# Optimization experiments

Measured on AMD Instinct MI355X. Metric: run time of the kernel, lower is better.

## Reference

```python
import jax, jax.numpy as jnp
import numpy as np

EPS = 1e-5

def _ln(x, g, b):
    mu = jnp.mean(x, axis=-1, keepdims=True)
    var = jnp.mean((x - mu) ** 2, axis=-1, keepdims=True)
    return (x - mu) * jax.lax.rsqrt(var + EPS) * g + b

def _lin(x, W, b):
    return x @ W + b

def setup_inputs() -> dict:
    B, D_IN, H = 32768, 512, 512
    key = jax.random.key(0)
    ks = jax.random.split(key, 20)
    def W(k, din, dout):
        return jax.random.normal(k, (din, dout), jnp.float32) / np.sqrt(din)
    inp = {
        'x': jax.random.normal(ks[0], (B, D_IN), jnp.float32),
        'h_prev': jax.random.normal(ks[1], (B, H), jnp.float32),
        's_prev': jax.random.normal(ks[2], (B, H), jnp.float32),
        'W_in': W(ks[3], D_IN, H), 'b_in': jnp.zeros((H,), jnp.float32),
        'g_ln_in': jnp.ones((H,), jnp.float32), 'b_ln_in': jnp.zeros((H,), jnp.float32),
        'g_ln_r': jnp.ones((H,), jnp.float32), 'b_ln_r': jnp.zeros((H,), jnp.float32),
        'g_ln_z': jnp.ones((H,), jnp.float32), 'b_ln_z': jnp.zeros((H,), jnp.float32),
        'g_ln_h': jnp.ones((H,), jnp.float32), 'b_ln_h': jnp.zeros((H,), jnp.float32),
        'W_r': W(ks[4], H, H), 'b_r': jnp.zeros((H,), jnp.float32),
        'W_z': W(ks[5], H, H), 'b_z': jnp.zeros((H,), jnp.float32),
        'W_k': W(ks[6], H, H), 'b_k': jnp.zeros((H,), jnp.float32),
        'W_v': W(ks[7], H, H), 'b_v': jnp.zeros((H,), jnp.float32),
        'W_h': W(ks[8], H, H), 'b_h': jnp.zeros((H,), jnp.float32),
        'W_d': W(ks[9], H, H), 'b_d': jnp.zeros((H,), jnp.float32),
    }
    return inp

def reference(x, h_prev, s_prev, W_in, b_in, g_ln_in, b_ln_in,
              g_ln_r, b_ln_r, g_ln_z, b_ln_z, g_ln_h, b_ln_h,
              W_r, b_r, W_z, b_z, W_k, b_k, W_v, b_v, W_h, b_h, W_d, b_d):
    # u = LN(input_proj(x))
    u = _ln(_lin(x, W_in, b_in), g_ln_in, b_ln_in)
    r = jax.nn.sigmoid(_ln(_lin(u, W_r, b_r), g_ln_r, b_ln_r))  # computed as in original (unused downstream)
    z = jax.nn.sigmoid(_ln(_lin(u, W_z, b_z), g_ln_z, b_ln_z))
    k = _lin(u, W_k, b_k)
    v = _lin(u, W_v, b_v)
    decay = jax.nn.sigmoid(_lin(u, W_d, b_d))
    s = decay * s_prev + k * v
    c = jnp.tanh(_ln(_lin(u + s, W_h, b_h), g_ln_h, b_ln_h))
    h = (1.0 - z) * c + z * h_prev
    return (h, s)
```

## Files before the change

kernel.cpp:

```cpp
#include <hip/hip_runtime.h>

typedef __attribute__((ext_vector_type(8))) short bf16x8;
typedef __attribute__((ext_vector_type(4))) float f32x4;

#define LN_EPS 1e-5f
#define MSZ ((size_t)32768 * 512)
#define WSZ ((size_t)512 * 512)

typedef const __attribute__((address_space(1))) void* gptr_t;
typedef __attribute__((address_space(3))) void* lptr_t;

__device__ __forceinline__ float b2f(unsigned short h) {
    unsigned int u = ((unsigned int)h) << 16;
    return __uint_as_float(u);
}
__device__ __forceinline__ short f2b(float f) {
    unsigned int u = __float_as_uint(f);
    unsigned int r = (u + 0x7FFFu + ((u >> 16) & 1u)) >> 16;
    return (short)(unsigned short)r;
}
__device__ __forceinline__ float sigmoid_f(float x) {
    return 1.0f / (1.0f + __expf(-x));
}
__device__ __forceinline__ float ldS(const void* p, size_t i, int isbf) {
    return isbf ? b2f(((const unsigned short*)p)[i]) : ((const float*)p)[i];
}
__device__ __forceinline__ void ld8(const void* p, size_t i, int isbf, float* o) {
    if (isbf) {
        bf16x8 v = *(const bf16x8*)((const unsigned short*)p + i);
        #pragma unroll
        for (int j = 0; j < 8; ++j) o[j] = b2f((unsigned short)v[j]);
    } else {
        f32x4 a = *(const f32x4*)((const float*)p + i);
        f32x4 b = *(const f32x4*)((const float*)p + i + 4);
        #pragma unroll
        for (int j = 0; j < 4; ++j) { o[j] = a[j]; o[4 + j] = b[j]; }
    }
}

__global__ void detect_dtype(const unsigned int* __restrict__ ones, int* __restrict__ flag) {
    if (threadIdx.x == 0 && blockIdx.x == 0)
        *flag = (ones[0] == 0x3F803F80u) ? 1 : 0;
}

__global__ __launch_bounds__(256) void transpose6(
    const void* __restrict__ s0, const void* __restrict__ s1,
    const void* __restrict__ s2, const void* __restrict__ s3,
    const void* __restrict__ s4, const void* __restrict__ s5,
    unsigned short* __restrict__ d0, unsigned short* __restrict__ d1,
    unsigned short* __restrict__ d2, unsigned short* __restrict__ d3,
    unsigned short* __restrict__ d4, unsigned short* __restrict__ d5,
    const int* __restrict__ flagp)
{
    const int isbf = *flagp;
    const void* srcs[6] = {s0, s1, s2, s3, s4, s5};
    unsigned short* dsts[6] = {d0, d1, d2, d3, d4, d5};
    const void* src = srcs[blockIdx.z];
    unsigned short* dst = dsts[blockIdx.z];

    __shared__ unsigned short tile[32][33];
    int tx = threadIdx.x, ty = threadIdx.y;
    int colbase = blockIdx.x * 32;
    int rowbase = blockIdx.y * 32;
    #pragma unroll
    for (int i = 0; i < 32; i += 8)
        tile[ty + i][tx] = (unsigned short)f2b(
            ldS(src, (size_t)(rowbase + ty + i) * 512 + colbase + tx, isbf));
    __syncthreads();
    #pragma unroll
    for (int i = 0; i < 32; i += 8)
        dst[(size_t)(colbase + ty + i) * 512 + rowbase + tx] = tile[tx][ty + i];
}

__global__ __launch_bounds__(256) void gemm_bt(
    const void* __restrict__ A,
    const unsigned short* __restrict__ BT,
    const void* __restrict__ bias0, const void* __restrict__ bias1,
    unsigned short* __restrict__ C0, unsigned short* __restrict__ C1,
    int nbshift, const int* __restrict__ flagp, int op, int araw,
    const void* __restrict__ s_prev,
    const unsigned short* __restrict__ kvb,
    const unsigned short* __restrict__ ubuf,
    void* __restrict__ dout)
{
    const int isbf = *flagp;
    const int K = 512;
    __shared__ unsigned short smem[128 * 136];
    unsigned short* As = smem;
    unsigned short* Bs = smem + 128 * 64;

    int t = threadIdx.x;
    int lane = t & 63;
    int wave = t >> 6;
    int wm = (wave >> 1) * 64;
    int wn = (wave & 1) * 64;

    int bflat = blockIdx.x;
    int xcd = bflat & 7;
    int bi = bflat >> 3;
    int n0 = (bi & ((1 << nbshift) - 1)) << 7;
    int mi = bi >> nbshift;
    int m0 = ((xcd << 5) + mi) << 7;

    int lr = lane >> 3;
    int lg = lane & 7;
    int gsrc = lg ^ lr;
    const unsigned short* Ab = (const unsigned short*)A;

    size_t a_off[4], b_off[4];
    #pragma unroll
    for (int i = 0; i < 4; ++i) {
        int c = wave * 4 + i;
        a_off[i] = (size_t)(m0 + 8 * c + lr) * K + gsrc * 8;
        b_off[i] = (size_t)(n0 + 8 * c + lr) * K + gsrc * 8;
    }

    int ml = lane & 15;
    int kg = lane >> 4;
    int sw = ml & 7;

    f32x4 acc[4][4] = {};

    const int doConv = (araw && !isbf);

    for (int k0 = 0; k0 < K; k0 += 64) {
        if (doConv) {
            const float* Af = (const float*)A;
            int r = t >> 1;
            #pragma unroll
            for (int j = 0; j < 4; ++j) {
                int G = (t & 1) * 4 + j;
                size_t gi = (size_t)(m0 + r) * K + k0 + G * 8;
                f32x4 lo = *(const f32x4*)&Af[gi];
                f32x4 hi = *(const f32x4*)&Af[gi + 4];
                bf16x8 p;
                #pragma unroll
                for (int z = 0; z < 4; ++z) { p[z] = f2b(lo[z]); p[4 + z] = f2b(hi[z]); }
                *(bf16x8*)&As[r * 64 + ((G ^ (r & 7)) * 8)] = p;
            }
        } else {
            #pragma unroll
            for (int i = 0; i < 4; ++i) {
                int c = wave * 4 + i;
                __builtin_amdgcn_global_load_lds(
                    (gptr_t)(const void*)(Ab + a_off[i] + k0),
                    (lptr_t)(void*)(As + c * 512), 16, 0, 0);
            }
        }
        #pragma unroll
        for (int i = 0; i < 4; ++i) {
            int c = wave * 4 + i;
            __builtin_amdgcn_global_load_lds(
                (gptr_t)(const void*)(BT + b_off[i] + k0),
                (lptr_t)(void*)(Bs + c * 512), 16, 0, 0);
        }
        __syncthreads();

        #pragma unroll
        for (int ks = 0; ks < 2; ++ks) {
            bf16x8 af[4], bfr[4];
            #pragma unroll
            for (int i = 0; i < 4; ++i) {
                int ga = ((ks << 2) + kg) ^ sw;
                af[i]  = *(const bf16x8*)&As[(wm + i * 16 + ml) * 64 + ga * 8];
                bfr[i] = *(const bf16x8*)&Bs[(wn + i * 16 + ml) * 64 + ga * 8];
            }
            #pragma unroll
            for (int i = 0; i < 4; ++i)
                #pragma unroll
                for (int j = 0; j < 4; ++j)
                    acc[i][j] = __builtin_amdgcn_mfma_f32_16x16x32_bf16(
                        af[i], bfr[j], acc[i][j], 0, 0, 0);
        }
        __syncthreads();
    }

    int seg = n0 >> 9;
    const void* bias = seg ? bias1 : bias0;
    unsigned short* Cs = seg ? C1 : C0;
    int ncol0 = n0 & 511;
    int cq = lane >> 4;
    int cl = lane & 15;
    #pragma unroll
    for (int j = 0; j < 4; ++j) {
        float bv = ldS(bias, ncol0 + wn + j * 16 + cl, isbf);
        #pragma unroll
        for (int i = 0; i < 4; ++i) {
            #pragma unroll
            for (int r = 0; r < 4; ++r) {
                float v = acc[i][j][r] + bv;
                if (op == 2) v = sigmoid_f(v);
                smem[(wm + i * 16 + cq * 4 + r) * 136 + wn + j * 16 + cl] =
                    (unsigned short)f2b(v);
            }
        }
    }
    __syncthreads();

    int tr = t >> 4;
    int tc = (t & 15) * 8;
    #pragma unroll
    for (int it = 0; it < 8; ++it) {
        int rl = it * 16 + tr;
        size_t idx = (size_t)(m0 + rl) * 512 + ncol0 + tc;
        bf16x8 v8 = *(bf16x8*)&smem[rl * 136 + tc];
        if (op == 0) {
            *(bf16x8*)&Cs[idx] = v8;
        } else if (op == 1) {
            bf16x8 k8 = *(const bf16x8*)&Cs[idx];
            bf16x8 o;
            #pragma unroll
            for (int z = 0; z < 8; ++z)
                o[z] = f2b(b2f((unsigned short)v8[z]) * b2f((unsigned short)k8[z]));
            *(bf16x8*)&Cs[idx] = o;
        } else {
            float sp[8];
            ld8(s_prev, idx, isbf, sp);
            bf16x8 kv8 = *(const bf16x8*)&kvb[idx];
            bf16x8 u8  = *(const bf16x8*)&ubuf[idx];
            float sv[8];
            bf16x8 a8;
            #pragma unroll
            for (int z = 0; z < 8; ++z) {
                sv[z] = b2f((unsigned short)v8[z]) * sp[z] + b2f((unsigned short)kv8[z]);
                a8[z] = f2b(b2f((unsigned short)u8[z]) + sv[z]);
            }
            if (isbf) {
                bf16x8 s8;
                #pragma unroll
                for (int z = 0; z < 8; ++z) s8[z] = f2b(sv[z]);
                *(bf16x8*)&((unsigned short*)dout)[MSZ + idx] = s8;
            } else {
                f32x4 lo, hi;
                #pragma unroll
                for (int z = 0; z < 4; ++z) { lo[z] = sv[z]; hi[z] = sv[4 + z]; }
                *(f32x4*)&((float*)dout)[MSZ + idx] = lo;
                *(f32x4*)&((float*)dout)[MSZ + idx + 4] = hi;
            }
            *(bf16x8*)&((unsigned short*)dout)[idx] = a8;
        }
    }
}

__global__ __launch_bounds__(256) void ln_rows(
    const unsigned short* __restrict__ X,
    const void* __restrict__ g,
    const void* __restrict__ b,
    unsigned short* __restrict__ Y,
    const int* __restrict__ flagp)
{
    const int isbf = *flagp;
    int wave = threadIdx.x >> 6, lane = threadIdx.x & 63;
    size_t row = (size_t)blockIdx.x * 4 + wave;
    size_t base = row * 512 + (size_t)lane * 8;

    bf16x8 xv = *(const bf16x8*)&X[base];
    float x[8];
    float s = 0.f, s2 = 0.f;
    #pragma unroll
    for (int i = 0; i < 8; ++i) {
        x[i] = b2f((unsigned short)xv[i]);
        s += x[i]; s2 += x[i] * x[i];
    }
    #pragma unroll
    for (int off = 32; off > 0; off >>= 1) {
        s  += __shfl_xor(s, off);
        s2 += __shfl_xor(s2, off);
    }
    float mu = s * (1.f / 512.f);
    float var = s2 * (1.f / 512.f) - mu * mu;
    float rs = rsqrtf(var + LN_EPS);

    float gv[8], bv[8];
    ld8(g, (size_t)lane * 8, isbf, gv);
    ld8(b, (size_t)lane * 8, isbf, bv);
    bf16x8 o;
    #pragma unroll
    for (int i = 0; i < 8; ++i)
        o[i] = f2b((x[i] - mu) * rs * gv[i] + bv[i]);
    *(bf16x8*)&Y[base] = o;
}

__global__ __launch_bounds__(256) void fused_out(
    const unsigned short* __restrict__ hlin,
    const unsigned short* __restrict__ zlin,
    const void* __restrict__ h_prev,
    const void* __restrict__ g_z, const void* __restrict__ b_z,
    const void* __restrict__ g_h, const void* __restrict__ b_h,
    void* __restrict__ dout,
    const int* __restrict__ flagp)
{
    const int isbf = *flagp;
    int wave = threadIdx.x >> 6, lane = threadIdx.x & 63;
    size_t row = (size_t)blockIdx.x * 4 + wave;
    size_t base = row * 512 + (size_t)lane * 8;

    bf16x8 zv8 = *(const bf16x8*)&zlin[base];
    bf16x8 hv8 = *(const bf16x8*)&hlin[base];
    float zf[8], hf[8];
    float sz = 0.f, sz2 = 0.f, sh = 0.f, sh2 = 0.f;
    #pragma unroll
    for (int i = 0; i < 8; ++i) {
        zf[i] = b2f((unsigned short)zv8[i]);
        hf[i] = b2f((unsigned short)hv8[i]);
        sz += zf[i]; sz2 += zf[i] * zf[i];
        sh += hf[i]; sh2 += hf[i] * hf[i];
    }
    #pragma unroll
    for (int off = 32; off > 0; off >>= 1) {
        sz  += __shfl_xor(sz, off);  sz2 += __shfl_xor(sz2, off);
        sh  += __shfl_xor(sh, off);  sh2 += __shfl_xor(sh2, off);
    }
    float muz = sz * (1.f / 512.f);
    float rsz = rsqrtf(sz2 * (1.f / 512.f) - muz * muz + LN_EPS);
    float muh = sh * (1.f / 512.f);
    float rsh = rsqrtf(sh2 * (1.f / 512.f) - muh * muh + LN_EPS);

    float gz[8], bz[8], gh[8], bh[8], hp[8];
    ld8(g_z, (size_t)lane * 8, isbf, gz);
    ld8(b_z, (size_t)lane * 8, isbf, bz);
    ld8(g_h, (size_t)lane * 8, isbf, gh);
    ld8(b_h, (size_t)lane * 8, isbf, bh);
    ld8(h_prev, base, isbf, hp);

    float hout[8];
    #pragma unroll
    for (int i = 0; i < 8; ++i) {
        float z = sigmoid_f((zf[i] - muz) * rsz * gz[i] + bz[i]);
        float c = tanhf((hf[i] - muh) * rsh * gh[i] + bh[i]);
        hout[i] = (1.f - z) * c + z * hp[i];
    }
    if (isbf) {
        bf16x8 o;
        #pragma unroll
        for (int i = 0; i < 8; ++i) o[i] = f2b(hout[i]);
        *(bf16x8*)&((unsigned short*)dout)[base] = o;
    } else {
        f32x4 a, b;
        #pragma unroll
        for (int i = 0; i < 4; ++i) { a[i] = hout[i]; b[i] = hout[4 + i]; }
        *(f32x4*)&((float*)dout)[base] = a;
        *(f32x4*)&((float*)dout)[base + 4] = b;
    }
}

extern "C" void kernel_launch(void* const* d_in, const int* in_sizes, int n_in,
                              void* d_out, int out_size, void* d_ws, size_t ws_size,
                              hipStream_t stream)
{
    (void)in_sizes; (void)n_in; (void)out_size; (void)ws_size;

    const void* x       = d_in[0];
    const void* h_prev  = d_in[1];
    const void* s_prev  = d_in[2];
    const void* W_in    = d_in[3];
    const void* b_in    = d_in[4];
    const void* g_ln_in = d_in[5];
    const void* b_ln_in = d_in[6];
    const void* g_ln_z  = d_in[9];
    const void* b_ln_z  = d_in[10];
    const void* g_ln_h  = d_in[11];
    const void* b_ln_h  = d_in[12];
    const void* W_z     = d_in[15];
    const void* b_z     = d_in[16];
    const void* W_k     = d_in[17];
    const void* b_k     = d_in[18];
    const void* W_v     = d_in[19];
    const void* b_v     = d_in[20];
    const void* W_h     = d_in[21];
    const void* b_h     = d_in[22];
    const void* W_d     = d_in[23];
    const void* b_d     = d_in[24];

    unsigned short* ws = (unsigned short*)d_ws;
    unsigned short* U  = ws;
    unsigned short* L  = ws + MSZ;
    unsigned short* Kb = ws + 2 * MSZ;
    unsigned short* WT = ws + 3 * MSZ;
    unsigned short* WT_in = WT;
    unsigned short* WT_z  = WT + 1 * WSZ;
    unsigned short* WT_k  = WT + 2 * WSZ;
    unsigned short* WT_v  = WT + 3 * WSZ;
    unsigned short* WT_d  = WT + 4 * WSZ;
    unsigned short* WT_h  = WT + 5 * WSZ;
    int* flag = (int*)(WT + 6 * WSZ);

    detect_dtype<<<1, 64, 0, stream>>>((const unsigned int*)g_ln_in, flag);
    transpose6<<<dim3(16, 16, 6), dim3(32, 8), 0, stream>>>(
        W_in, W_z, W_k, W_v, W_d, W_h,
        WT_in, WT_z, WT_k, WT_v, WT_d, WT_h, flag);

    gemm_bt<<<1024, 256, 0, stream>>>(x, WT_in, b_in, nullptr, L, nullptr,
                                      2, flag, 0, 1,
                                      nullptr, nullptr, nullptr, nullptr);
    ln_rows<<<8192, 256, 0, stream>>>(L, g_ln_in, b_ln_in, U, flag);
    gemm_bt<<<2048, 256, 0, stream>>>(U, WT_z, b_z, b_k, L, Kb,
                                      3, flag, 0, 0,
                                      nullptr, nullptr, nullptr, nullptr);
    gemm_bt<<<1024, 256, 0, stream>>>(U, WT_v, b_v, nullptr, Kb, nullptr,
                                      2, flag, 1, 0,
                                      nullptr, nullptr, nullptr, nullptr);
    gemm_bt<<<1024, 256, 0, stream>>>(U, WT_d, b_d, nullptr, nullptr, nullptr,
                                      2, flag, 2, 0,
                                      s_prev, Kb, U, d_out);
    gemm_bt<<<1024, 256, 0, stream>>>(d_out, WT_h, b_h, nullptr, Kb, nullptr,
                                      2, flag, 0, 0,
                                      nullptr, nullptr, nullptr, nullptr);
    fused_out<<<8192, 256, 0, stream>>>(Kb, L, h_prev,
                                        g_ln_z, b_ln_z, g_ln_h, b_ln_h,
                                        d_out, flag);
}
```

Measured before the change: 539.9 us.

## Merge z/k/v/d GEMMs into one launch and split elementwise state update

Moves the fp32-to-bf16 conversion of x into a separate pre-pass kernel, so the GEMM always uses the direct global-to-LDS load path. The four projections z, k, v and d are computed in a single wide GEMM launch (N=2048) writing to four buffers, replacing three launches that had fused epilogues. The decay sigmoid, the state update s and the u+s computation move into a standalone elementwise kernel. This cuts launches and reuses the A tiles, at the cost of extra bf16 intermediate traffic (V and D buffers written and read back, plus the converted x).

```diff
diff --git a/kernel.cpp b/kernel.cpp
--- a/kernel.cpp
+++ b/kernel.cpp
@@ -72,22 +72,36 @@
         dst[(size_t)(colbase + ty + i) * 512 + rowbase + tx] = tile[tx][ty + i];
 }
 
+__global__ __launch_bounds__(256) void cvt_x(
+    const float* __restrict__ x, unsigned short* __restrict__ Xb,
+    const int* __restrict__ flagp)
+{
+    if (*flagp) return;
+    size_t i = ((size_t)blockIdx.x * 256 + threadIdx.x) * 8;
+    f32x4 a = *(const f32x4*)&x[i];
+    f32x4 b = *(const f32x4*)&x[i + 4];
+    bf16x8 o;
+    #pragma unroll
+    for (int j = 0; j < 4; ++j) { o[j] = f2b(a[j]); o[4 + j] = f2b(b[j]); }
+    *(bf16x8*)&Xb[i] = o;
+}
+
 __global__ __launch_bounds__(256) void gemm_bt(
-    const void* __restrict__ A,
+    const void* __restrict__ Araw, const unsigned short* __restrict__ Aconv,
     const unsigned short* __restrict__ BT,
-    const void* __restrict__ bias0, const void* __restrict__ bias1,
+    const void* __restrict__ b0, const void* __restrict__ b1,
+    const void* __restrict__ b2, const void* __restrict__ b3,
     unsigned short* __restrict__ C0, unsigned short* __restrict__ C1,
-    int nbshift, const int* __restrict__ flagp, int op, int araw,
-    const void* __restrict__ s_prev,
-    const unsigned short* __restrict__ kvb,
-    const unsigned short* __restrict__ ubuf,
-    void* __restrict__ dout)
+    unsigned short* __restrict__ C2, unsigned short* __restrict__ C3,
+    int nbshift, const int* __restrict__ flagp)
 {
     const int isbf = *flagp;
     const int K = 512;
     __shared__ unsigned short smem[128 * 136];
     unsigned short* As = smem;
     unsigned short* Bs = smem + 128 * 64;
+
+    const unsigned short* Ab = isbf ? (const unsigned short*)Araw : Aconv;
 
     int t = threadIdx.x;
     int lane = t & 63;
@@ -105,7 +119,6 @@
     int lr = lane >> 3;
     int lg = lane & 7;
     int gsrc = lg ^ lr;
-    const unsigned short* Ab = (const unsigned short*)A;
 
     size_t a_off[4], b_off[4];
     #pragma unroll
@@ -121,31 +134,13 @@
 
     f32x4 acc[4][4] = {};
 
-    const int doConv = (araw && !isbf);
-
     for (int k0 = 0; k0 < K; k0 += 64) {
-        if (doConv) {
-            const float* Af = (const float*)A;
-            int r = t >> 1;
-            #pragma unroll
-            for (int j = 0; j < 4; ++j) {
-                int G = (t & 1) * 4 + j;
-                size_t gi = (size_t)(m0 + r) * K + k0 + G * 8;
-                f32x4 lo = *(const f32x4*)&Af[gi];
-                f32x4 hi = *(const f32x4*)&Af[gi + 4];
-                bf16x8 p;
-                #pragma unroll
-                for (int z = 0; z < 4; ++z) { p[z] = f2b(lo[z]); p[4 + z] = f2b(hi[z]); }
-                *(bf16x8*)&As[r * 64 + ((G ^ (r & 7)) * 8)] = p;
-            }
-        } else {
-            #pragma unroll
-            for (int i = 0; i < 4; ++i) {
-                int c = wave * 4 + i;
-                __builtin_amdgcn_global_load_lds(
-                    (gptr_t)(const void*)(Ab + a_off[i] + k0),
-                    (lptr_t)(void*)(As + c * 512), 16, 0, 0);
-            }
+        #pragma unroll
+        for (int i = 0; i < 4; ++i) {
+            int c = wave * 4 + i;
+            __builtin_amdgcn_global_load_lds(
+                (gptr_t)(const void*)(Ab + a_off[i] + k0),
+                (lptr_t)(void*)(As + c * 512), 16, 0, 0);
         }
         #pragma unroll
         for (int i = 0; i < 4; ++i) {
@@ -176,8 +171,8 @@
     }
 
     int seg = n0 >> 9;
-    const void* bias = seg ? bias1 : bias0;
-    unsigned short* Cs = seg ? C1 : C0;
+    const void* bias = (seg == 0) ? b0 : (seg == 1) ? b1 : (seg == 2) ? b2 : b3;
+    unsigned short* Cs = (seg == 0) ? C0 : (seg == 1) ? C1 : (seg == 2) ? C2 : C3;
     int ncol0 = n0 & 511;
     int cq = lane >> 4;
     int cl = lane & 15;
@@ -188,10 +183,8 @@
         for (int i = 0; i < 4; ++i) {
             #pragma unroll
             for (int r = 0; r < 4; ++r) {
-                float v = acc[i][j][r] + bv;
-                if (op == 2) v = sigmoid_f(v);
                 smem[(wm + i * 16 + cq * 4 + r) * 136 + wn + j * 16 + cl] =
-                    (unsigned short)f2b(v);
+                    (unsigned short)f2b(acc[i][j][r] + bv);
             }
         }
     }
@@ -203,43 +196,49 @@
     for (int it = 0; it < 8; ++it) {
         int rl = it * 16 + tr;
         size_t idx = (size_t)(m0 + rl) * 512 + ncol0 + tc;
-        bf16x8 v8 = *(bf16x8*)&smem[rl * 136 + tc];
-        if (op == 0) {
-            *(bf16x8*)&Cs[idx] = v8;
-        } else if (op == 1) {
-            bf16x8 k8 = *(const bf16x8*)&Cs[idx];
-            bf16x8 o;
-            #pragma unroll
-            for (int z = 0; z < 8; ++z)
-                o[z] = f2b(b2f((unsigned short)v8[z]) * b2f((unsigned short)k8[z]));
-            *(bf16x8*)&Cs[idx] = o;
-        } else {
-            float sp[8];
-            ld8(s_prev, idx, isbf, sp);
-            bf16x8 kv8 = *(const bf16x8*)&kvb[idx];
-            bf16x8 u8  = *(const bf16x8*)&ubuf[idx];
-            float sv[8];
-            bf16x8 a8;
-            #pragma unroll
-            for (int z = 0; z < 8; ++z) {
-                sv[z] = b2f((unsigned short)v8[z]) * sp[z] + b2f((unsigned short)kv8[z]);
-                a8[z] = f2b(b2f((unsigned short)u8[z]) + sv[z]);
-            }
-            if (isbf) {
-                bf16x8 s8;
-                #pragma unroll
-                for (int z = 0; z < 8; ++z) s8[z] = f2b(sv[z]);
-                *(bf16x8*)&((unsigned short*)dout)[MSZ + idx] = s8;
-            } else {
-                f32x4 lo, hi;
-                #pragma unroll
-                for (int z = 0; z < 4; ++z) { lo[z] = sv[z]; hi[z] = sv[4 + z]; }
-                *(f32x4*)&((float*)dout)[MSZ + idx] = lo;
-                *(f32x4*)&((float*)dout)[MSZ + idx + 4] = hi;
-            }
-            *(bf16x8*)&((unsigned short*)dout)[idx] = a8;
-        }
-    }
+        *(bf16x8*)&Cs[idx] = *(bf16x8*)&smem[rl * 136 + tc];
+    }
+}
+
+__global__ __launch_bounds__(256) void fused_sa(
+    const unsigned short* __restrict__ klin,
+    const unsigned short* __restrict__ vlin,
+    const unsigned short* __restrict__ dlin,
+    const unsigned short* __restrict__ u,
+    const void* __restrict__ s_prev,
+    void* __restrict__ dout,
+    const int* __restrict__ flagp)
+{
+    const int isbf = *flagp;
+    size_t i = ((size_t)blockIdx.x * 256 + threadIdx.x) * 8;
+    bf16x8 k8 = *(const bf16x8*)&klin[i];
+    bf16x8 v8 = *(const bf16x8*)&vlin[i];
+    bf16x8 d8 = *(const bf16x8*)&dlin[i];
+    bf16x8 u8 = *(const bf16x8*)&u[i];
+    float sp[8];
+    ld8(s_prev, i, isbf, sp);
+
+    float sv[8];
+    bf16x8 a8;
+    #pragma unroll
+    for (int z = 0; z < 8; ++z) {
+        float dv = sigmoid_f(b2f((unsigned short)d8[z]));
+        sv[z] = dv * sp[z] + b2f((unsigned short)k8[z]) * b2f((unsigned short)v8[z]);
+        a8[z] = f2b(b2f((unsigned short)u8[z]) + sv[z]);
+    }
+    if (isbf) {
+        bf16x8 s8;
+        #pragma unroll
+        for (int z = 0; z < 8; ++z) s8[z] = f2b(sv[z]);
+        *(bf16x8*)&((unsigned short*)dout)[MSZ + i] = s8;
+    } else {
+        f32x4 lo, hi;
+        #pragma unroll
+        for (int z = 0; z < 4; ++z) { lo[z] = sv[z]; hi[z] = sv[4 + z]; }
+        *(f32x4*)&((float*)dout)[MSZ + i] = lo;
+        *(f32x4*)&((float*)dout)[MSZ + i + 4] = hi;
+    }
+    *(bf16x8*)&((unsigned short*)dout)[i] = a8;
 }
 
 __global__ __launch_bounds__(256) void ln_rows(
@@ -376,7 +375,9 @@
     unsigned short* U  = ws;
     unsigned short* L  = ws + MSZ;
     unsigned short* Kb = ws + 2 * MSZ;
-    unsigned short* WT = ws + 3 * MSZ;
+    unsigned short* Vb = ws + 3 * MSZ;
+    unsigned short* Db = ws + 4 * MSZ;
+    unsigned short* WT = ws + 5 * MSZ;
     unsigned short* WT_in = WT;
     unsigned short* WT_z  = WT + 1 * WSZ;
     unsigned short* WT_k  = WT + 2 * WSZ;
@@ -390,22 +391,23 @@
         W_in, W_z, W_k, W_v, W_d, W_h,
         WT_in, WT_z, WT_k, WT_v, WT_d, WT_h, flag);
 
-    gemm_bt<<<1024, 256, 0, stream>>>(x, WT_in, b_in, nullptr, L, nullptr,
-                                      2, flag, 0, 1,
-                                      nullptr, nullptr, nullptr, nullptr);
+    cvt_x<<<8192, 256, 0, stream>>>((const float*)x, Vb, flag);
+
+    gemm_bt<<<1024, 256, 0, stream>>>(x, Vb, WT_in,
+                                      b_in, b_in, b_in, b_in,
+                                      L, L, L, L, 2, flag);
     ln_rows<<<8192, 256, 0, stream>>>(L, g_ln_in, b_ln_in, U, flag);
-    gemm_bt<<<2048, 256, 0, stream>>>(U, WT_z, b_z, b_k, L, Kb,
-                                      3, flag, 0, 0,
-                                      nullptr, nullptr, nullptr, nullptr);
-    gemm_bt<<<1024, 256, 0, stream>>>(U, WT_v, b_v, nullptr, Kb, nullptr,
-                                      2, flag, 1, 0,
-                                      nullptr, nullptr, nullptr, nullptr);
-    gemm_bt<<<1024, 256, 0, stream>>>(U, WT_d, b_d, nullptr, nullptr, nullptr,
-                                      2, flag, 2, 0,
-                                      s_prev, Kb, U, d_out);
-    gemm_bt<<<1024, 256, 0, stream>>>(d_out, WT_h, b_h, nullptr, Kb, nullptr,
-                                      2, flag, 0, 0,
-                                      nullptr, nullptr, nullptr, nullptr);
+
+    gemm_bt<<<4096, 256, 0, stream>>>(U, U, WT_z,
+                                      b_z, b_k, b_v, b_d,
+                                      L, Kb, Vb, Db, 4, flag);
+
+    fused_sa<<<8192, 256, 0, stream>>>(Kb, Vb, Db, U, s_prev, d_out, flag);
+
+    gemm_bt<<<1024, 256, 0, stream>>>(d_out, (const unsigned short*)d_out, WT_h,
+                                      b_h, b_h, b_h, b_h,
+                                      Kb, Kb, Kb, Kb, 2, flag);
+
     fused_out<<<8192, 256, 0, stream>>>(Kb, L, h_prev,
                                         g_ln_z, b_ln_z, g_ln_h, b_ln_h,
                                         d_out, flag);
```

Result: faster. 524.2 us (-2.9%).

## Fuse LayerNorms into full-row GEMMs and merge z/k/v/d projections

Applied to the files above, without the earlier changes.

Replaces the chain of seven GEMM and elementwise launches with three kernels. A full-row GEMM (64 rows × 512 cols per block, 512 threads) applies the input LayerNorm in its epilogue, and a second instance fuses the final z/h LayerNorms, gating and output. A new kernel computes the z, k, v and d projections together (relying on the contiguous transposed weights) and forms s and u+s in its epilogue. This removes the intermediate bf16 round trips through global memory and extra launches, at the cost of larger LDS use, lower occupancy and smaller per-wave tiles in the merged GEMM.

```diff
diff --git a/kernel.cpp b/kernel.cpp
--- a/kernel.cpp
+++ b/kernel.cpp
@@ -72,99 +72,80 @@
         dst[(size_t)(colbase + ty + i) * 512 + rowbase + tx] = tile[tx][ty + i];
 }
 
-__global__ __launch_bounds__(256) void gemm_bt(
-    const void* __restrict__ A,
+template<int OUT, bool CONV>
+__global__ __launch_bounds__(512) void gemm_row(
+    const void* __restrict__ Araw,
     const unsigned short* __restrict__ BT,
-    const void* __restrict__ bias0, const void* __restrict__ bias1,
-    unsigned short* __restrict__ C0, unsigned short* __restrict__ C1,
-    int nbshift, const int* __restrict__ flagp, int op, int araw,
-    const void* __restrict__ s_prev,
-    const unsigned short* __restrict__ kvb,
-    const unsigned short* __restrict__ ubuf,
-    void* __restrict__ dout)
+    const void* __restrict__ bias,
+    const void* __restrict__ g0, const void* __restrict__ b0v,
+    const void* __restrict__ g1, const void* __restrict__ b1v,
+    const unsigned short* __restrict__ zlin,
+    const void* __restrict__ h_prev,
+    void* __restrict__ out,
+    const int* __restrict__ flagp)
 {
     const int isbf = *flagp;
     const int K = 512;
-    __shared__ unsigned short smem[128 * 136];
+    __shared__ unsigned short smem[36864];
     unsigned short* As = smem;
-    unsigned short* Bs = smem + 128 * 64;
+    unsigned short* Bs = smem + 64 * 64;
 
     int t = threadIdx.x;
     int lane = t & 63;
     int wave = t >> 6;
-    int wm = (wave >> 1) * 64;
-    int wn = (wave & 1) * 64;
-
-    int bflat = blockIdx.x;
-    int xcd = bflat & 7;
-    int bi = bflat >> 3;
-    int n0 = (bi & ((1 << nbshift) - 1)) << 7;
-    int mi = bi >> nbshift;
-    int m0 = ((xcd << 5) + mi) << 7;
-
-    int lr = lane >> 3;
-    int lg = lane & 7;
-    int gsrc = lg ^ lr;
-    const unsigned short* Ab = (const unsigned short*)A;
-
-    size_t a_off[4], b_off[4];
-    #pragma unroll
-    for (int i = 0; i < 4; ++i) {
-        int c = wave * 4 + i;
-        a_off[i] = (size_t)(m0 + 8 * c + lr) * K + gsrc * 8;
-        b_off[i] = (size_t)(n0 + 8 * c + lr) * K + gsrc * 8;
-    }
-
-    int ml = lane & 15;
-    int kg = lane >> 4;
-    int sw = ml & 7;
+    int wn = wave * 64;
+
+    int b = blockIdx.x;
+    int m0 = ((b & 7) * 64 + (b >> 3)) * 64;
+
+    int lr = lane >> 3, lg = lane & 7, gsrc = lg ^ lr;
+    const unsigned short* Ab = (const unsigned short*)Araw;
+
+    size_t a_off = (size_t)(m0 + 8 * wave + lr) * K + gsrc * 8;
+    size_t b_off[8];
+    #pragma unroll
+    for (int i = 0; i < 8; ++i)
+        b_off[i] = (size_t)(64 * wave + 8 * i + lr) * K + gsrc * 8;
+
+    int cr = t >> 3, cg = t & 7;
+
+    int ml = lane & 15, kg = lane >> 4, sw = ml & 7;
 
     f32x4 acc[4][4] = {};
-
-    const int doConv = (araw && !isbf);
+    const bool conv_now = CONV && !isbf;
 
     for (int k0 = 0; k0 < K; k0 += 64) {
-        if (doConv) {
-            const float* Af = (const float*)A;
-            int r = t >> 1;
-            #pragma unroll
-            for (int j = 0; j < 4; ++j) {
-                int G = (t & 1) * 4 + j;
-                size_t gi = (size_t)(m0 + r) * K + k0 + G * 8;
-                f32x4 lo = *(const f32x4*)&Af[gi];
-                f32x4 hi = *(const f32x4*)&Af[gi + 4];
-                bf16x8 p;
-                #pragma unroll
-                for (int z = 0; z < 4; ++z) { p[z] = f2b(lo[z]); p[4 + z] = f2b(hi[z]); }
-                *(bf16x8*)&As[r * 64 + ((G ^ (r & 7)) * 8)] = p;
-            }
+        if (conv_now) {
+            const float* Af = (const float*)Araw;
+            size_t gi = (size_t)(m0 + cr) * K + k0 + cg * 8;
+            f32x4 lo = *(const f32x4*)&Af[gi];
+            f32x4 hi = *(const f32x4*)&Af[gi + 4];
+            bf16x8 p;
+            #pragma unroll
+            for (int z = 0; z < 4; ++z) { p[z] = f2b(lo[z]); p[4 + z] = f2b(hi[z]); }
+            *(bf16x8*)&As[cr * 64 + ((cg ^ (cr & 7)) * 8)] = p;
         } else {
-            #pragma unroll
-            for (int i = 0; i < 4; ++i) {
-                int c = wave * 4 + i;
-                __builtin_amdgcn_global_load_lds(
-                    (gptr_t)(const void*)(Ab + a_off[i] + k0),
-                    (lptr_t)(void*)(As + c * 512), 16, 0, 0);
-            }
-        }
-        #pragma unroll
-        for (int i = 0; i < 4; ++i) {
-            int c = wave * 4 + i;
+            __builtin_amdgcn_global_load_lds(
+                (gptr_t)(const void*)(Ab + a_off + k0),
+                (lptr_t)(void*)(As + wave * 512), 16, 0, 0);
+        }
+        #pragma unroll
+        for (int i = 0; i < 8; ++i)
             __builtin_amdgcn_global_load_lds(
                 (gptr_t)(const void*)(BT + b_off[i] + k0),
-                (lptr_t)(void*)(Bs + c * 512), 16, 0, 0);
-        }
+                (lptr_t)(void*)(Bs + (wave * 8 + i) * 512), 16, 0, 0);
         __syncthreads();
 
         #pragma unroll
         for (int ks = 0; ks < 2; ++ks) {
+            int ga = ((ks << 2) + kg) ^ sw;
             bf16x8 af[4], bfr[4];
             #pragma unroll
-            for (int i = 0; i < 4; ++i) {
-                int ga = ((ks << 2) + kg) ^ sw;
-                af[i]  = *(const bf16x8*)&As[(wm + i * 16 + ml) * 64 + ga * 8];
-                bfr[i] = *(const bf16x8*)&Bs[(wn + i * 16 + ml) * 64 + ga * 8];
-            }
+            for (int i = 0; i < 4; ++i)
+                af[i] = *(const bf16x8*)&As[(i * 16 + ml) * 64 + ga * 8];
+            #pragma unroll
+            for (int j = 0; j < 4; ++j)
+                bfr[j] = *(const bf16x8*)&Bs[(wn + j * 16 + ml) * 64 + ga * 8];
             #pragma unroll
             for (int i = 0; i < 4; ++i)
                 #pragma unroll
@@ -175,172 +156,233 @@
         __syncthreads();
     }
 
-    int seg = n0 >> 9;
-    const void* bias = seg ? bias1 : bias0;
-    unsigned short* Cs = seg ? C1 : C0;
-    int ncol0 = n0 & 511;
-    int cq = lane >> 4;
-    int cl = lane & 15;
+    unsigned short* E = smem;
+    int cq = lane >> 4, cl = lane & 15;
     #pragma unroll
     for (int j = 0; j < 4; ++j) {
-        float bv = ldS(bias, ncol0 + wn + j * 16 + cl, isbf);
-        #pragma unroll
-        for (int i = 0; i < 4; ++i) {
-            #pragma unroll
-            for (int r = 0; r < 4; ++r) {
-                float v = acc[i][j][r] + bv;
-                if (op == 2) v = sigmoid_f(v);
-                smem[(wm + i * 16 + cq * 4 + r) * 136 + wn + j * 16 + cl] =
-                    (unsigned short)f2b(v);
-            }
-        }
+        float bv = ldS(bias, wn + j * 16 + cl, isbf);
+        #pragma unroll
+        for (int i = 0; i < 4; ++i)
+            #pragma unroll
+            for (int r = 0; r < 4; ++r)
+                E[(i * 16 + cq * 4 + r) * 520 + wn + j * 16 + cl] =
+                    (unsigned short)f2b(acc[i][j][r] + bv);
     }
     __syncthreads();
 
-    int tr = t >> 4;
-    int tc = (t & 15) * 8;
-    #pragma unroll
-    for (int it = 0; it < 8; ++it) {
-        int rl = it * 16 + tr;
-        size_t idx = (size_t)(m0 + rl) * 512 + ncol0 + tc;
-        bf16x8 v8 = *(bf16x8*)&smem[rl * 136 + tc];
-        if (op == 0) {
-            *(bf16x8*)&Cs[idx] = v8;
-        } else if (op == 1) {
-            bf16x8 k8 = *(const bf16x8*)&Cs[idx];
+    if (OUT == 0) {
+        float gv[8], bv[8];
+        ld8(g0, (size_t)lane * 8, isbf, gv);
+        ld8(b0v, (size_t)lane * 8, isbf, bv);
+        #pragma unroll
+        for (int q = 0; q < 8; ++q) {
+            int r = wave * 8 + q;
+            bf16x8 xv = *(const bf16x8*)&E[r * 520 + lane * 8];
+            float x[8], s = 0.f, s2 = 0.f;
+            #pragma unroll
+            for (int i = 0; i < 8; ++i) {
+                x[i] = b2f((unsigned short)xv[i]);
+                s += x[i]; s2 += x[i] * x[i];
+            }
+            #pragma unroll
+            for (int off = 32; off > 0; off >>= 1) {
+                s += __shfl_xor(s, off); s2 += __shfl_xor(s2, off);
+            }
+            float mu = s * (1.f / 512.f);
+            float rs = rsqrtf(s2 * (1.f / 512.f) - mu * mu + LN_EPS);
             bf16x8 o;
             #pragma unroll
-            for (int z = 0; z < 8; ++z)
-                o[z] = f2b(b2f((unsigned short)v8[z]) * b2f((unsigned short)k8[z]));
-            *(bf16x8*)&Cs[idx] = o;
-        } else {
-            float sp[8];
-            ld8(s_prev, idx, isbf, sp);
-            bf16x8 kv8 = *(const bf16x8*)&kvb[idx];
-            bf16x8 u8  = *(const bf16x8*)&ubuf[idx];
-            float sv[8];
-            bf16x8 a8;
-            #pragma unroll
-            for (int z = 0; z < 8; ++z) {
-                sv[z] = b2f((unsigned short)v8[z]) * sp[z] + b2f((unsigned short)kv8[z]);
-                a8[z] = f2b(b2f((unsigned short)u8[z]) + sv[z]);
+            for (int i = 0; i < 8; ++i)
+                o[i] = f2b((x[i] - mu) * rs * gv[i] + bv[i]);
+            *(bf16x8*)&((unsigned short*)out)[(size_t)(m0 + r) * 512 + lane * 8] = o;
+        }
+    } else {
+        float gh[8], bh[8], gz[8], bz[8];
+        ld8(g0, (size_t)lane * 8, isbf, gh);
+        ld8(b0v, (size_t)lane * 8, isbf, bh);
+        ld8(g1, (size_t)lane * 8, isbf, gz);
+        ld8(b1v, (size_t)lane * 8, isbf, bz);
+        #pragma unroll
+        for (int q = 0; q < 8; ++q) {
+            int r = wave * 8 + q;
+            size_t base = (size_t)(m0 + r) * 512 + lane * 8;
+            bf16x8 hv8 = *(const bf16x8*)&E[r * 520 + lane * 8];
+            bf16x8 zv8 = *(const bf16x8*)&zlin[base];
+            float hf[8], zf[8];
+            float sh = 0.f, sh2 = 0.f, sz = 0.f, sz2 = 0.f;
+            #pragma unroll
+            for (int i = 0; i < 8; ++i) {
+                hf[i] = b2f((unsigned short)hv8[i]);
+                zf[i] = b2f((unsigned short)zv8[i]);
+                sh += hf[i]; sh2 += hf[i] * hf[i];
+                sz += zf[i]; sz2 += zf[i] * zf[i];
+            }
+            #pragma unroll
+            for (int off = 32; off > 0; off >>= 1) {
+                sh += __shfl_xor(sh, off); sh2 += __shfl_xor(sh2, off);
+                sz += __shfl_xor(sz, off); sz2 += __shfl_xor(sz2, off);
+            }
+            float muh = sh * (1.f / 512.f);
+            float rsh = rsqrtf(sh2 * (1.f / 512.f) - muh * muh + LN_EPS);
+            float muz = sz * (1.f / 512.f);
+            float rsz = rsqrtf(sz2 * (1.f / 512.f) - muz * muz + LN_EPS);
+            float hp[8];
+            ld8(h_prev, base, isbf, hp);
+            float hout[8];
+            #pragma unroll
+            for (int i = 0; i < 8; ++i) {
+                float z = sigmoid_f((zf[i] - muz) * rsz * gz[i] + bz[i]);
+                float c = tanhf((hf[i] - muh) * rsh * gh[i] + bh[i]);
+                hout[i] = (1.f - z) * c + z * hp[i];
             }
             if (isbf) {
-                bf16x8 s8;
+                bf16x8 o;
                 #pragma unroll
-                for (int z = 0; z < 8; ++z) s8[z] = f2b(sv[z]);
-                *(bf16x8*)&((unsigned short*)dout)[MSZ + idx] = s8;
+                for (int i = 0; i < 8; ++i) o[i] = f2b(hout[i]);
+                *(bf16x8*)&((unsigned short*)out)[base] = o;
             } else {
                 f32x4 lo, hi;
                 #pragma unroll
-                for (int z = 0; z < 4; ++z) { lo[z] = sv[z]; hi[z] = sv[4 + z]; }
-                *(f32x4*)&((float*)dout)[MSZ + idx] = lo;
-                *(f32x4*)&((float*)dout)[MSZ + idx + 4] = hi;
-            }
-            *(bf16x8*)&((unsigned short*)dout)[idx] = a8;
-        }
-    }
-}
-
-__global__ __launch_bounds__(256) void ln_rows(
-    const unsigned short* __restrict__ X,
-    const void* __restrict__ g,
-    const void* __restrict__ b,
-    unsigned short* __restrict__ Y,
-    const int* __restrict__ flagp)
-{
-    const int isbf = *flagp;
-    int wave = threadIdx.x >> 6, lane = threadIdx.x & 63;
-    size_t row = (size_t)blockIdx.x * 4 + wave;
-    size_t base = row * 512 + (size_t)lane * 8;
-
-    bf16x8 xv = *(const bf16x8*)&X[base];
-    float x[8];
-    float s = 0.f, s2 = 0.f;
-    #pragma unroll
-    for (int i = 0; i < 8; ++i) {
-        x[i] = b2f((unsigned short)xv[i]);
-        s += x[i]; s2 += x[i] * x[i];
-    }
-    #pragma unroll
-    for (int off = 32; off > 0; off >>= 1) {
-        s  += __shfl_xor(s, off);
-        s2 += __shfl_xor(s2, off);
-    }
-    float mu = s * (1.f / 512.f);
-    float var = s2 * (1.f / 512.f) - mu * mu;
-    float rs = rsqrtf(var + LN_EPS);
-
-    float gv[8], bv[8];
-    ld8(g, (size_t)lane * 8, isbf, gv);
-    ld8(b, (size_t)lane * 8, isbf, bv);
-    bf16x8 o;
-    #pragma unroll
-    for (int i = 0; i < 8; ++i)
-        o[i] = f2b((x[i] - mu) * rs * gv[i] + bv[i]);
-    *(bf16x8*)&Y[base] = o;
-}
-
-__global__ __launch_bounds__(256) void fused_out(
-    const unsigned short* __restrict__ hlin,
-    const unsigned short* __restrict__ zlin,
-    const void* __restrict__ h_prev,
-    const void* __restrict__ g_z, const void* __restrict__ b_z,
-    const void* __restrict__ g_h, const void* __restrict__ b_h,
+                for (int i = 0; i < 4; ++i) { lo[i] = hout[i]; hi[i] = hout[4 + i]; }
+                *(f32x4*)&((float*)out)[base] = lo;
+                *(f32x4*)&((float*)out)[base + 4] = hi;
+            }
+        }
+    }
+}
+
+__global__ __launch_bounds__(256) void gemm_zkvd(
+    const unsigned short* __restrict__ U,
+    const unsigned short* __restrict__ BT,
+    const void* __restrict__ bz, const void* __restrict__ bk,
+    const void* __restrict__ bv_, const void* __restrict__ bd,
+    const void* __restrict__ s_prev,
+    unsigned short* __restrict__ zout,
+    unsigned short* __restrict__ aout,
     void* __restrict__ dout,
     const int* __restrict__ flagp)
 {
     const int isbf = *flagp;
-    int wave = threadIdx.x >> 6, lane = threadIdx.x & 63;
-    size_t row = (size_t)blockIdx.x * 4 + wave;
-    size_t base = row * 512 + (size_t)lane * 8;
-
-    bf16x8 zv8 = *(const bf16x8*)&zlin[base];
-    bf16x8 hv8 = *(const bf16x8*)&hlin[base];
-    float zf[8], hf[8];
-    float sz = 0.f, sz2 = 0.f, sh = 0.f, sh2 = 0.f;
-    #pragma unroll
-    for (int i = 0; i < 8; ++i) {
-        zf[i] = b2f((unsigned short)zv8[i]);
-        hf[i] = b2f((unsigned short)hv8[i]);
-        sz += zf[i]; sz2 += zf[i] * zf[i];
-        sh += hf[i]; sh2 += hf[i] * hf[i];
-    }
-    #pragma unroll
-    for (int off = 32; off > 0; off >>= 1) {
-        sz  += __shfl_xor(sz, off);  sz2 += __shfl_xor(sz2, off);
-        sh  += __shfl_xor(sh, off);  sh2 += __shfl_xor(sh2, off);
-    }
-    float muz = sz * (1.f / 512.f);
-    float rsz = rsqrtf(sz2 * (1.f / 512.f) - muz * muz + LN_EPS);
-    float muh = sh * (1.f / 512.f);
-    float rsh = rsqrtf(sh2 * (1.f / 512.f) - muh * muh + LN_EPS);
-
-    float gz[8], bz[8], gh[8], bh[8], hp[8];
-    ld8(g_z, (size_t)lane * 8, isbf, gz);
-    ld8(b_z, (size_t)lane * 8, isbf, bz);
-    ld8(g_h, (size_t)lane * 8, isbf, gh);
-    ld8(b_h, (size_t)lane * 8, isbf, bh);
-    ld8(h_prev, base, isbf, hp);
-
-    float hout[8];
-    #pragma unroll
-    for (int i = 0; i < 8; ++i) {
-        float z = sigmoid_f((zf[i] - muz) * rsz * gz[i] + bz[i]);
-        float c = tanhf((hf[i] - muh) * rsh * gh[i] + bh[i]);
-        hout[i] = (1.f - z) * c + z * hp[i];
-    }
-    if (isbf) {
-        bf16x8 o;
-        #pragma unroll
-        for (int i = 0; i < 8; ++i) o[i] = f2b(hout[i]);
-        *(bf16x8*)&((unsigned short*)dout)[base] = o;
-    } else {
-        f32x4 a, b;
-        #pragma unroll
-        for (int i = 0; i < 4; ++i) { a[i] = hout[i]; b[i] = hout[4 + i]; }
-        *(f32x4*)&((float*)dout)[base] = a;
-        *(f32x4*)&((float*)dout)[base + 4] = b;
+    const int K = 512;
+    __shared__ unsigned short smem[20480];
+    unsigned short* As = smem;
+
+    int t = threadIdx.x;
+    int lane = t & 63;
+    int wave = t >> 6;
+    int wm = (wave >> 1) * 32;
+    int wn = (wave & 1) * 32;
+
+    int b = blockIdx.x;
+    int xcd = b & 7;
+    int bi = b >> 3;
+    int nb = bi & 7;
+    int mi = bi >> 3;
+    int m0 = (xcd * 64 + mi) * 64;
+    int nc0 = nb * 64;
+
+    int lr = lane >> 3, lg = lane & 7, gsrc = lg ^ lr;
+
+    size_t a_off[2], b_off[8];
+    #pragma unroll
+    for (int i = 0; i < 2; ++i)
+        a_off[i] = (size_t)(m0 + 8 * (2 * wave + i) + lr) * K + gsrc * 8;
+    #pragma unroll
+    for (int i = 0; i < 8; ++i)
+        b_off[i] = (size_t)(wave * 512 + nc0 + 8 * i + lr) * K + gsrc * 8;
+
+    int ml = lane & 15, kg = lane >> 4, sw = ml & 7;
+
+    f32x4 acc[4][2][2] = {};
+
+    for (int k0 = 0; k0 < K; k0 += 64) {
+        #pragma unroll
+        for (int i = 0; i < 2; ++i)
+            __builtin_amdgcn_global_load_lds(
+                (gptr_t)(const void*)(U + a_off[i] + k0),
+                (lptr_t)(void*)(As + (2 * wave + i) * 512), 16, 0, 0);
+        #pragma unroll
+        for (int i = 0; i < 8; ++i)
+            __builtin_amdgcn_global_load_lds(
+                (gptr_t)(const void*)(BT + b_off[i] + k0),
+                (lptr_t)(void*)(smem + 4096 + wave * 4096 + i * 512), 16, 0, 0);
+        __syncthreads();
+
+        #pragma unroll
+        for (int ks = 0; ks < 2; ++ks) {
+            int ga = ((ks << 2) + kg) ^ sw;
+            bf16x8 af[2];
+            #pragma unroll
+            for (int i = 0; i < 2; ++i)
+                af[i] = *(const bf16x8*)&As[(wm + i * 16 + ml) * 64 + ga * 8];
+            #pragma unroll
+            for (int s = 0; s < 4; ++s) {
+                bf16x8 bf0 = *(const bf16x8*)&smem[4096 + s * 4096 + (wn + ml) * 64 + ga * 8];
+                bf16x8 bf1 = *(const bf16x8*)&smem[4096 + s * 4096 + (wn + 16 + ml) * 64 + ga * 8];
+                #pragma unroll
+                for (int i = 0; i < 2; ++i) {
+                    acc[s][i][0] = __builtin_amdgcn_mfma_f32_16x16x32_bf16(
+                        af[i], bf0, acc[s][i][0], 0, 0, 0);
+                    acc[s][i][1] = __builtin_amdgcn_mfma_f32_16x16x32_bf16(
+                        af[i], bf1, acc[s][i][1], 0, 0, 0);
+                }
+            }
+        }
+        __syncthreads();
+    }
+
+    int cq = lane >> 4, cl = lane & 15;
+    const void* biases[4] = {bz, bk, bv_, bd};
+    #pragma unroll
+    for (int s = 0; s < 4; ++s) {
+        #pragma unroll
+        for (int j = 0; j < 2; ++j) {
+            float bvv = ldS(biases[s], nc0 + wn + j * 16 + cl, isbf);
+            #pragma unroll
+            for (int i = 0; i < 2; ++i)
+                #pragma unroll
+                for (int r = 0; r < 4; ++r)
+                    smem[s * 4608 + (wm + i * 16 + cq * 4 + r) * 72 + wn + j * 16 + cl] =
+                        (unsigned short)f2b(acc[s][i][j][r] + bvv);
+        }
+    }
+    __syncthreads();
+
+    int r = t >> 2;
+    int c0 = (t & 3) * 16;
+    #pragma unroll
+    for (int g = 0; g < 2; ++g) {
+        int col = c0 + g * 8;
+        size_t idx = (size_t)(m0 + r) * 512 + nc0 + col;
+        bf16x8 z8 = *(const bf16x8*)&smem[0 * 4608 + r * 72 + col];
+        bf16x8 k8 = *(const bf16x8*)&smem[1 * 4608 + r * 72 + col];
+        bf16x8 v8 = *(const bf16x8*)&smem[2 * 4608 + r * 72 + col];
+        bf16x8 d8 = *(const bf16x8*)&smem[3 * 4608 + r * 72 + col];
+        bf16x8 u8 = *(const bf16x8*)&U[idx];
+        float sp[8];
+        ld8(s_prev, idx, isbf, sp);
+        float sv[8];
+        bf16x8 a8;
+        #pragma unroll
+        for (int z = 0; z < 8; ++z) {
+            float dv = sigmoid_f(b2f((unsigned short)d8[z]));
+            sv[z] = dv * sp[z] + b2f((unsigned short)k8[z]) * b2f((unsigned short)v8[z]);
+            a8[z] = f2b(b2f((unsigned short)u8[z]) + sv[z]);
+        }
+        *(bf16x8*)&zout[idx] = z8;
+        *(bf16x8*)&aout[idx] = a8;
+        if (isbf) {
+            bf16x8 s8;
+            #pragma unroll
+            for (int z = 0; z < 8; ++z) s8[z] = f2b(sv[z]);
+            *(bf16x8*)&((unsigned short*)dout)[MSZ + idx] = s8;
+        } else {
+            f32x4 lo, hi;
+            #pragma unroll
+            for (int z = 0; z < 4; ++z) { lo[z] = sv[z]; hi[z] = sv[4 + z]; }
+            *(f32x4*)&((float*)dout)[MSZ + idx] = lo;
+            *(f32x4*)&((float*)dout)[MSZ + idx + 4] = hi;
+        }
     }
 }
 
@@ -375,7 +417,7 @@
     unsigned short* ws = (unsigned short*)d_ws;
     unsigned short* U  = ws;
     unsigned short* L  = ws + MSZ;
-    unsigned short* Kb = ws + 2 * MSZ;
+    unsigned short* Ab = ws + 2 * MSZ;
     unsigned short* WT = ws + 3 * MSZ;
     unsigned short* WT_in = WT;
     unsigned short* WT_z  = WT + 1 * WSZ;
@@ -384,29 +426,22 @@
     unsigned short* WT_d  = WT + 4 * WSZ;
     unsigned short* WT_h  = WT + 5 * WSZ;
     int* flag = (int*)(WT + 6 * WSZ);
+    (void)WT_k; (void)WT_v; (void)WT_d;
 
     detect_dtype<<<1, 64, 0, stream>>>((const unsigned int*)g_ln_in, flag);
     transpose6<<<dim3(16, 16, 6), dim3(32, 8), 0, stream>>>(
         W_in, W_z, W_k, W_v, W_d, W_h,
         WT_in, WT_z, WT_k, WT_v, WT_d, WT_h, flag);
 
-    gemm_bt<<<1024, 256, 0, stream>>>(x, WT_in, b_in, nullptr, L, nullptr,
-                                      2, flag, 0, 1,
-                                      nullptr, nullptr, nullptr, nullptr);
-    ln_rows<<<8192, 256, 0, stream>>>(L, g_ln_in, b_ln_in, U, flag);
-    gemm_bt<<<2048, 256, 0, stream>>>(U, WT_z, b_z, b_k, L, Kb,
-                                      3, flag, 0, 0,
-                                      nullptr, nullptr, nullptr, nullptr);
-    gemm_bt<<<1024, 256, 0, stream>>>(U, WT_v, b_v, nullptr, Kb, nullptr,
-                                      2, flag, 1, 0,
-                                      nullptr, nullptr, nullptr, nullptr);
-    gemm_bt<<<1024, 256, 0, stream>>>(U, WT_d, b_d, nullptr, nullptr, nullptr,
-                                      2, flag, 2, 0,
-                                      s_prev, Kb, U, d_out);
-    gemm_bt<<<1024, 256, 0, stream>>>(d_out, WT_h, b_h, nullptr, Kb, nullptr,
-                                      2, flag, 0, 0,
-                                      nullptr, nullptr, nullptr, nullptr);
-    fused_out<<<8192, 256, 0, stream>>>(Kb, L, h_prev,
-                                        g_ln_z, b_ln_z, g_ln_h, b_ln_h,
-                                        d_out, flag);
-}
+    gemm_row<0, true><<<512, 512, 0, stream>>>(
+        x, WT_in, b_in, g_ln_in, b_ln_in,
+        nullptr, nullptr, nullptr, nullptr, U, flag);
+
+    gemm_zkvd<<<4096, 256, 0, stream>>>(
+        U, WT_z, b_z, b_k, b_v, b_d,
+        s_prev, L, Ab, d_out, flag);
+
+    gemm_row<1, false><<<512, 512, 0, stream>>>(
+        Ab, WT_h, b_h, g_ln_h, b_ln_h,
+        g_ln_z, b_ln_z, L, h_prev, d_out, flag);
+}
```

Result: faster. 458.0 us (-15.2%).
